# Optimization experiments

Measured on AMD Instinct MI355X. Metric: run time of the kernel, lower is better.

## Reference

```python
import jax, jax.numpy as jnp
import numpy as np
from jax import lax

EPS = 1e-6
CLAMP = 1e4


def _ln_last(x, w, b):
    # fp32 LayerNorm over last dim
    mu = jnp.mean(x, axis=-1, keepdims=True)
    var = jnp.mean(jnp.square(x - mu), axis=-1, keepdims=True)
    return (x - mu) * lax.rsqrt(var + EPS) * w + b


def _nan_clean(x):
    return jnp.nan_to_num(x, nan=0.0, posinf=CLAMP, neginf=-CLAMP)


def setup_inputs() -> dict:
    key = jax.random.key(0)
    B, C, H, W = 4, 256, 64, 64
    hid = 2 * C  # expand=2
    k = 3        # d_conv
    ks = jax.random.split(key, 12)
    s = 0.02
    return {
        "x": jax.random.normal(ks[0], (B, C, H, W), jnp.float32),
        "ln2d_w": jnp.ones((C,), jnp.float32),
        "ln2d_b": jnp.zeros((C,), jnp.float32),
        "inproj_w": jax.random.normal(ks[1], (C, C), jnp.float32) * s,
        "inproj_b": jnp.zeros((C,), jnp.float32),
        "dw2d_w": jax.random.normal(ks[2], (C, 3, 3), jnp.float32) * s,
        "dw2d_b": jnp.zeros((C,), jnp.float32),
        "ssm_ln_w": jnp.ones((C,), jnp.float32),
        "ssm_ln_b": jnp.zeros((C,), jnp.float32),
        "ssm_in_w": jax.random.normal(ks[3], (2 * hid, C), jnp.float32) * s,
        "ssm_in_b": jnp.zeros((2 * hid,), jnp.float32),
        "ssm_dw_w": jax.random.normal(ks[4], (hid, k), jnp.float32) * s,
        "ssm_dw_b": jnp.zeros((hid,), jnp.float32),
        "ssm_out_w": jax.random.normal(ks[5], (C, hid), jnp.float32) * s,
        "ssm_out_b": jnp.zeros((C,), jnp.float32),
        "outproj_w": jax.random.normal(ks[6], (C, C), jnp.float32) * s,
        "outproj_b": jnp.zeros((C,), jnp.float32),
    }


def reference(x, ln2d_w, ln2d_b, inproj_w, inproj_b, dw2d_w, dw2d_b,
              ssm_ln_w, ssm_ln_b, ssm_in_w, ssm_in_b, ssm_dw_w, ssm_dw_b,
              ssm_out_w, ssm_out_b, outproj_w, outproj_b):
    B, C, H, W = x.shape
    L = H * W

    # LN2d over channel dim (per-pixel LN on C)
    y = _ln_last(x.transpose(0, 2, 3, 1), ln2d_w, ln2d_b).transpose(0, 3, 1, 2)

    # 1x1 conv in_proj
    y = jnp.einsum('bchw,oc->bohw', y, inproj_w) + inproj_b[None, :, None, None]

    # depthwise 3x3 conv, SAME padding
    y = lax.conv_general_dilated(
        y, dw2d_w[:, None, :, :], (1, 1), ((1, 1), (1, 1)),
        dimension_numbers=('NCHW', 'OIHW', 'NCHW'),
        feature_group_count=C) + dw2d_b[None, :, None, None]

    # cross-scan: 4 routes (B,L,C)
    s0 = y.reshape(B, C, L).transpose(0, 2, 1)                      # row-major
    s1 = s0[:, ::-1]                                                # reversed
    s2 = y.transpose(0, 1, 3, 2).reshape(B, C, L).transpose(0, 2, 1)  # col-major
    s3 = s2[:, ::-1]
    s = jnp.concatenate([s0, s1, s2, s3], axis=0)  # (4B, L, C), shared SSM weights

    # MambaOrLite fallback: LN -> GLU -> depthwise conv1d -> out proj + residual
    r = _ln_last(s, ssm_ln_w, ssm_ln_b)
    r = r @ ssm_in_w.T + ssm_in_b                   # (4B, L, 2*hid)
    a, g = jnp.split(r, 2, axis=-1)
    r = a * jax.nn.sigmoid(g)                       # (4B, L, hid)
    r = r.transpose(0, 2, 1)                        # (4B, hid, L)
    hid = r.shape[1]
    k = ssm_dw_w.shape[-1]
    pad = ((k - 1) // 2, k // 2)
    r = lax.conv_general_dilated(
        r, ssm_dw_w[:, None, :], (1,), (pad,),
        dimension_numbers=('NCH', 'OIH', 'NCH'),
        feature_group_count=hid) + ssm_dw_b[None, :, None]
    r = r.transpose(0, 2, 1) @ ssm_out_w.T + ssm_out_b  # (4B, L, C)
    ys = _nan_clean(r) + s

    # cross-merge: average the 4 routes back to (B,C,H,W)
    y0, y1, y2, y3 = jnp.split(ys, 4, axis=0)
    m0 = y0.transpose(0, 2, 1).reshape(B, C, H, W)
    m1 = y1[:, ::-1].transpose(0, 2, 1).reshape(B, C, H, W)
    m2 = y2.transpose(0, 2, 1).reshape(B, C, W, H).transpose(0, 1, 3, 2)
    m3 = y3[:, ::-1].transpose(0, 2, 1).reshape(B, C, W, H).transpose(0, 1, 3, 2)
    m = (m0 + m1 + m2 + m3) * 0.25

    out = jnp.einsum('bchw,oc->bohw', m, outproj_w) + outproj_b[None, :, None, None]
    out = _nan_clean(out)
    return out + x
```

## Files before the change

kernel.cpp:

```cpp
#include <hip/hip_runtime.h>

typedef float f32x4 __attribute__((ext_vector_type(4)));
typedef __bf16 bf16x8 __attribute__((ext_vector_type(8)));
typedef unsigned short u16;
typedef unsigned int u32;

__device__ __forceinline__ float bf2f(u32 b) {
  u32 x = (b & 0xffffu) << 16;
  return __builtin_bit_cast(float, x);
}
__device__ __forceinline__ u16 f2bf(float f) {
  u32 x = __builtin_bit_cast(u32, f);
  x += 0x7fffu + ((x >> 16) & 1u);
  return (u16)(x >> 16);
}
__device__ __forceinline__ void gload16(const void* g, void* l) {
  __builtin_amdgcn_global_load_lds((__attribute__((address_space(1))) void*)g,
                                   (__attribute__((address_space(3))) void*)l,
                                   16, 0, 0);
}
__device__ __forceinline__ int xcd_swz(int bid, int nwg) {
  int per = nwg >> 3;
  return (bid & 7) * per + (bid >> 3);
}

__global__ __launch_bounds__(256, 2)
void k_ln2d_prep(const float* __restrict__ x, const float* __restrict__ lw,
                 const float* __restrict__ lb, u16* __restrict__ A,
                 const float* __restrict__ inproj_w, const float* __restrict__ ssm_in_w,
                 const float* __restrict__ ssm_out_w, const float* __restrict__ outproj_w,
                 const float* __restrict__ dw2d_w, const float* __restrict__ ssm_dw_w,
                 const float* __restrict__ ssm_dw_b, const float* __restrict__ ssm_out_b,
                 u16* __restrict__ w1b, u16* __restrict__ w2b, u16* __restrict__ w3b,
                 u16* __restrict__ w4b, float* __restrict__ cvec, float* __restrict__ wT9,
                 float* __restrict__ w02, float* __restrict__ w14) {
  __shared__ float T[256 * 65];
  __shared__ float ps1[4][64], ps2[4][64];
  __shared__ float mu[64], rsd[64];
  int bid = blockIdx.x, tid = threadIdx.x;
  if (bid >= 256) {
    int pb = bid - 256;
    if (pb < 512) {
      const float* s; u16* d; int base;
      if (pb < 256)      { s = ssm_in_w;  d = w2b; base = pb; }
      else if (pb < 384) { s = ssm_out_w; d = w3b; base = pb - 256; }
      else if (pb < 448) { s = inproj_w;  d = w1b; base = pb - 384; }
      else               { s = outproj_w; d = w4b; base = pb - 448; }
      int i = base * 1024 + tid * 4;
      float4 v = *(const float4*)&s[i];
      u32 a = (u32)f2bf(v.x) | ((u32)f2bf(v.y) << 16);
      u32 b = (u32)f2bf(v.z) | ((u32)f2bf(v.w) << 16);
      *(uint2*)&d[i] = make_uint2(a, b);
    } else if (pb == 512) {
      float s = ssm_out_b[tid];
      const float* wr = ssm_out_w + (size_t)tid * 512;
      #pragma unroll 8
      for (int k = 0; k < 512; ++k) s += ssm_dw_b[k] * wr[k];
      cvec[tid] = s;
    } else {
      #pragma unroll
      for (int j = 0; j < 9; ++j) wT9[j * 256 + tid] = dw2d_w[tid * 9 + j];
      #pragma unroll
      for (int q = 0; q < 2; ++q) {
        int c = tid + q * 256;
        w02[c] = ssm_dw_w[c * 3 + 0] + ssm_dw_w[c * 3 + 2];
        w14[c] = 4.f * ssm_dw_w[c * 3 + 1];
      }
    }
    return;
  }
  int wv = tid >> 6, lane = tid & 63;
  int cq = lane >> 4, p4 = (lane & 15) * 4;
  int n0 = bid * 64, bb = n0 >> 12, hw0 = n0 & 4095;
  const float* xb = x + ((size_t)bb << 20);
  float s0 = 0, s1 = 0, s2 = 0, s3 = 0;
  float q0 = 0, q1 = 0, q2 = 0, q3 = 0;
  #pragma unroll 4
  for (int i = 0; i < 16; ++i) {
    int c = wv * 64 + i * 4 + cq;
    float4 v = *(const float4*)&xb[((size_t)c << 12) + hw0 + p4];
    T[c * 65 + p4 + 0] = v.x; T[c * 65 + p4 + 1] = v.y;
    T[c * 65 + p4 + 2] = v.z; T[c * 65 + p4 + 3] = v.w;
    s0 += v.x; s1 += v.y; s2 += v.z; s3 += v.w;
    q0 += v.x * v.x; q1 += v.y * v.y; q2 += v.z * v.z; q3 += v.w * v.w;
  }
  #pragma unroll
  for (int off = 16; off < 64; off <<= 1) {
    s0 += __shfl_xor(s0, off); s1 += __shfl_xor(s1, off);
    s2 += __shfl_xor(s2, off); s3 += __shfl_xor(s3, off);
    q0 += __shfl_xor(q0, off); q1 += __shfl_xor(q1, off);
    q2 += __shfl_xor(q2, off); q3 += __shfl_xor(q3, off);
  }
  if (cq == 0) {
    ps1[wv][p4 + 0] = s0; ps1[wv][p4 + 1] = s1; ps1[wv][p4 + 2] = s2; ps1[wv][p4 + 3] = s3;
    ps2[wv][p4 + 0] = q0; ps2[wv][p4 + 1] = q1; ps2[wv][p4 + 2] = q2; ps2[wv][p4 + 3] = q3;
  }
  __syncthreads();
  if (tid < 64) {
    float S1 = ps1[0][tid] + ps1[1][tid] + ps1[2][tid] + ps1[3][tid];
    float S2 = ps2[0][tid] + ps2[1][tid] + ps2[2][tid] + ps2[3][tid];
    float m = S1 * (1.f / 256.f);
    float var = S2 * (1.f / 256.f) - m * m;
    mu[tid] = m;
    rsd[tid] = rsqrtf(var + 1e-6f);
  }
  __syncthreads();
  int c4b = (tid & 15) * 4, p2b = tid >> 4;
  #pragma unroll
  for (int cc = 0; cc < 4; ++cc) {
    int c4 = cc * 64 + c4b;
    float4 w4 = *(const float4*)&lw[c4];
    float4 g4 = *(const float4*)&lb[c4];
    #pragma unroll
    for (int i2 = 0; i2 < 4; ++i2) {
      int p2 = p2b + 16 * i2;
      float m = mu[p2], rs = rsd[p2];
      float o0 = (T[(c4 + 0) * 65 + p2] - m) * rs * w4.x + g4.x;
      float o1 = (T[(c4 + 1) * 65 + p2] - m) * rs * w4.y + g4.y;
      float o2 = (T[(c4 + 2) * 65 + p2] - m) * rs * w4.z + g4.z;
      float o3 = (T[(c4 + 3) * 65 + p2] - m) * rs * w4.w + g4.w;
      u32 a = (u32)f2bf(o0) | ((u32)f2bf(o1) << 16);
      u32 b = (u32)f2bf(o2) | ((u32)f2bf(o3) << 16);
      *(uint2*)&A[(size_t)(n0 + p2) * 256 + c4] = make_uint2(a, b);
    }
  }
}

__global__ __launch_bounds__(256)
void k_dw3x3_ln(const u16* __restrict__ Y1, const float* __restrict__ wT,
                const float* __restrict__ dwb, const float* __restrict__ lnw,
                const float* __restrict__ lnb, u16* __restrict__ Yc,
                u16* __restrict__ A) {
  int tid = threadIdx.x;
  int wg = xcd_swz(blockIdx.x, 4096);
  int n = wg * 4 + (tid >> 6);
  int lane = tid & 63;
  int c0 = lane * 4;
  int b = n >> 12, hw = n & 4095, h = hw >> 6, w = hw & 63;
  float4 b4 = *(const float4*)&dwb[c0];
  float a0 = b4.x, a1 = b4.y, a2 = b4.z, a3 = b4.w;
  #pragma unroll
  for (int ky = 0; ky < 3; ++ky) {
    int hh = h + ky - 1;
    if (hh < 0 || hh > 63) continue;
    #pragma unroll
    for (int kx = 0; kx < 3; ++kx) {
      int ww = w + kx - 1;
      if (ww < 0 || ww > 63) continue;
      size_t nn = ((size_t)b << 12) + (hh << 6) + ww;
      uint2 u = *(const uint2*)&Y1[nn * 256 + c0];
      float4 w4 = *(const float4*)&wT[(ky * 3 + kx) * 256 + c0];
      a0 += bf2f(u.x) * w4.x;
      a1 += bf2f(u.x >> 16) * w4.y;
      a2 += bf2f(u.y) * w4.z;
      a3 += bf2f(u.y >> 16) * w4.w;
    }
  }
  u32 p0 = (u32)f2bf(a0) | ((u32)f2bf(a1) << 16);
  u32 p1 = (u32)f2bf(a2) | ((u32)f2bf(a3) << 16);
  *(uint2*)&Yc[(size_t)n * 256 + c0] = make_uint2(p0, p1);
  float s1 = a0 + a1 + a2 + a3;
  float s2 = a0 * a0 + a1 * a1 + a2 * a2 + a3 * a3;
  #pragma unroll
  for (int off = 1; off < 64; off <<= 1) {
    s1 += __shfl_xor(s1, off);
    s2 += __shfl_xor(s2, off);
  }
  float m = s1 * (1.f / 256.f);
  float var = s2 * (1.f / 256.f) - m * m;
  float rs = rsqrtf(var + 1e-6f);
  float4 w4 = *(const float4*)&lnw[c0];
  float4 g4 = *(const float4*)&lnb[c0];
  float o0 = (a0 - m) * rs * w4.x + g4.x;
  float o1 = (a1 - m) * rs * w4.y + g4.y;
  float o2 = (a2 - m) * rs * w4.z + g4.z;
  float o3 = (a3 - m) * rs * w4.w + g4.w;
  u32 qa = (u32)f2bf(o0) | ((u32)f2bf(o1) << 16);
  u32 qb = (u32)f2bf(o2) | ((u32)f2bf(o3) << 16);
  *(uint2*)&A[(size_t)n * 256 + c0] = make_uint2(qa, qb);
}

template <int EPI, int NCT, bool RFAST>
__global__ __launch_bounds__(256, 4)
void k_gemm2(const u16* __restrict__ R, const u16* __restrict__ Cm,
             const float* __restrict__ bias, int K, int ldo,
             u16* __restrict__ outb, float* __restrict__ outf,
             const float* __restrict__ resf) {
  __shared__ u16 tR[2][64 * 32];
  __shared__ u16 tC[2][128 * 32];
  int tid = threadIdx.x, lane = tid & 63, wv = tid >> 6;
  int wg = xcd_swz(blockIdx.x, gridDim.x);
  int nRt = gridDim.x / NCT;
  int rt = RFAST ? (wg % nRt) : (wg / NCT);
  int ct = RFAST ? (wg / nRt) : (wg % NCT);
  int r0 = rt * 64, c0 = ct * 128;
  int fr = lane & 15, kc = lane >> 4;
  int sr = lane >> 2, sc = (lane & 3) * 8;
  f32x4 acc[4][2] = {};
  int nK = K >> 5;
  const u16* gR  = R  + (size_t)(r0 + wv * 16 + sr) * K + sc;
  const u16* gC0 = Cm + (size_t)(c0 + wv * 32 + sr) * K + sc;
  const u16* gC1 = Cm + (size_t)(c0 + wv * 32 + 16 + sr) * K + sc;
  auto STAGE = [&](int buf, int kt) {
    int k0 = kt * 32;
    gload16(gR + k0,  &tR[buf][wv * 16 * 32]);
    gload16(gC0 + k0, &tC[buf][(wv * 32) * 32]);
    gload16(gC1 + k0, &tC[buf][(wv * 32 + 16) * 32]);
  };
  auto COMPUTE = [&](int buf) {
    bf16x8 af[4], wf[2];
    #pragma unroll
    for (int m = 0; m < 4; ++m)
      af[m] = *(const bf16x8*)&tR[buf][(m * 16 + fr) * 32 + kc * 8];
    #pragma unroll
    for (int n = 0; n < 2; ++n)
      wf[n] = *(const bf16x8*)&tC[buf][(wv * 32 + n * 16 + fr) * 32 + kc * 8];
    #pragma unroll
    for (int m = 0; m < 4; ++m)
      #pragma unroll
      for (int n = 0; n < 2; ++n)
        acc[m][n] = __builtin_amdgcn_mfma_f32_16x16x32_bf16(af[m], wf[n], acc[m][n], 0, 0, 0);
  };
  STAGE(0, 0);
  __syncthreads();
  int cur = 0;
  for (int kt = 0; kt < nK - 1; ++kt) {
    STAGE(cur ^ 1, kt + 1);
    __builtin_amdgcn_sched_barrier(0);
    COMPUTE(cur);
    __syncthreads();
    cur ^= 1;
  }
  COMPUTE(cur);
  #pragma unroll
  for (int m = 0; m < 4; ++m) {
    #pragma unroll
    for (int n = 0; n < 2; ++n) {
      #pragma unroll
      for (int r = 0; r < 4; ++r) {
        float v = acc[m][n][r];
        if (EPI == 0) {
          int gn = r0 + m * 16 + kc * 4 + r;
          int go = c0 + wv * 32 + n * 16 + fr;
          outb[(size_t)gn * ldo + go] = f2bf(v + bias[go]);
        } else {
          int go = r0 + m * 16 + kc * 4 + r;
          int gn = c0 + wv * 32 + n * 16 + fr;
          int b = gn >> 12, hw = gn & 4095;
          size_t idx = (((size_t)(b * 256 + go)) << 12) + hw;
          float res = __builtin_nontemporal_load(&resf[idx]);
          __builtin_nontemporal_store(v + bias[go] + res, &outf[idx]);
        }
      }
    }
  }
}

__global__ __launch_bounds__(256, 2)
void k_gate2(const u16* __restrict__ A, const u16* __restrict__ W,
             const float* __restrict__ bias, u16* __restrict__ G) {
  __shared__ u16 tR[2][128 * 32];
  __shared__ u16 tCa[2][128 * 32];
  __shared__ u16 tCg[2][128 * 32];
  int tid = threadIdx.x, lane = tid & 63, wv = tid >> 6;
  int wg = xcd_swz(blockIdx.x, 512);
  int rt = wg >> 2, ot = wg & 3;
  int r0 = rt * 128, o0 = ot * 128;
  int wr = wv >> 1, wc = wv & 1;
  int fr = lane & 15, kc = lane >> 4;
  const int K = 256;
  f32x4 acca[4][4] = {}, accg[4][4] = {};
  auto STAGE = [&](int buf, int kt) {
    int k0 = kt * 32;
    #pragma unroll
    for (int i = 0; i < 2; ++i) {
      int s0 = wv * 128 + i * 64;
      int s = s0 + lane;
      int row = s >> 2, off = (s & 3) * 8;
      gload16(A + (size_t)(r0 + row) * K + k0 + off, &tR[buf][s0 * 8]);
      gload16(W + (size_t)(o0 + row) * K + k0 + off, &tCa[buf][s0 * 8]);
      gload16(W + (size_t)(512 + o0 + row) * K + k0 + off, &tCg[buf][s0 * 8]);
    }
  };
  auto COMPUTE = [&](int buf) {
    bf16x8 af[4], wa[4], wgf[4];
    #pragma unroll
    for (int m = 0; m < 4; ++m)
      af[m] = *(const bf16x8*)&tR[buf][(wr * 64 + m * 16 + fr) * 32 + kc * 8];
    #pragma unroll
    for (int n = 0; n < 4; ++n) {
      wa[n]  = *(const bf16x8*)&tCa[buf][(wc * 64 + n * 16 + fr) * 32 + kc * 8];
      wgf[n] = *(const bf16x8*)&tCg[buf][(wc * 64 + n * 16 + fr) * 32 + kc * 8];
    }
    #pragma unroll
    for (int m = 0; m < 4; ++m)
      #pragma unroll
      for (int n = 0; n < 4; ++n) {
        acca[m][n] = __builtin_amdgcn_mfma_f32_16x16x32_bf16(af[m], wa[n], acca[m][n], 0, 0, 0);
        accg[m][n] = __builtin_amdgcn_mfma_f32_16x16x32_bf16(af[m], wgf[n], accg[m][n], 0, 0, 0);
      }
  };
  STAGE(0, 0);
  __syncthreads();
  int cur = 0;
  for (int kt = 0; kt < 7; ++kt) {
    STAGE(cur ^ 1, kt + 1);
    __builtin_amdgcn_sched_barrier(0);
    COMPUTE(cur);
    __syncthreads();
    cur ^= 1;
  }
  COMPUTE(cur);
  #pragma unroll
  for (int m = 0; m < 4; ++m) {
    #pragma unroll
    for (int n = 0; n < 4; ++n) {
      #pragma unroll
      for (int r = 0; r < 4; ++r) {
        int gn = r0 + wr * 64 + m * 16 + kc * 4 + r;
        int go = o0 + wc * 64 + n * 16 + fr;
        float a = acca[m][n][r] + bias[go];
        float g = accg[m][n][r] + bias[512 + go];
        G[(size_t)gn * 512 + go] = f2bf(a / (1.f + expf(-g)));
      }
    }
  }
}

__global__ __launch_bounds__(256, 2)
void k_gemm_scan(const u16* __restrict__ G, const u16* __restrict__ W3,
                 const float* __restrict__ w02, const float* __restrict__ w14,
                 const float* __restrict__ cvec, const u16* __restrict__ Yc,
                 u16* __restrict__ M) {
  __shared__ u16 tR[2][32 * 32];
  __shared__ u16 tC[2][256 * 32];
  int tid = threadIdx.x, lane = tid & 63, wv = tid >> 6;
  int wg = xcd_swz(blockIdx.x, 512);
  int r0 = wg * 32;
  int fr = lane & 15, kc = lane >> 4;
  int zrow = tid >> 3;
  int zg = (tid & 7) * 4;
  int n = r0 + zrow;
  int b = n >> 12, hw = n & 4095, h = hw >> 6, w = hw & 63;
  int m = w * 64 + h;
  int mm1 = m - 1, mp1 = m + 1;
  size_t o_c = (size_t)n * 512 + zg;
  size_t o_p = (size_t)(hw > 0 ? n - 1 : n) * 512 + zg;
  size_t o_n = (size_t)(hw < 4095 ? n + 1 : n) * 512 + zg;
  size_t o_u = (size_t)(m > 0 ? ((b << 12) + ((mm1 & 63) << 6) + (mm1 >> 6)) : n) * 512 + zg;
  size_t o_d = (size_t)(m < 4095 ? ((b << 12) + ((mp1 & 63) << 6) + (mp1 >> 6)) : n) * 512 + zg;
  float mP = hw > 0 ? 1.f : 0.f, mN = hw < 4095 ? 1.f : 0.f;
  float mU = m > 0 ? 1.f : 0.f, mD = m < 4095 ? 1.f : 0.f;
  f32x4 acc[2][4] = {};
  auto STAGE_C = [&](int buf, int kt) {
    int k0 = kt * 32;
    #pragma unroll
    for (int i = 0; i < 4; ++i) {
      int s0 = wv * 256 + i * 64;
      int s = s0 + lane;
      int row = s >> 2, off = (s & 3) * 8;
      gload16(W3 + (size_t)row * 512 + k0 + off, &tC[buf][s0 * 8]);
    }
  };
  uint2 lc, lp, ln_, lu, ld;
  float4 va, vb;
  auto ZLOAD = [&](int kt) {
    int c = kt * 32 + zg;
    lc  = *(const uint2*)&G[o_c + (kt * 32)];
    lp  = *(const uint2*)&G[o_p + (kt * 32)];
    ln_ = *(const uint2*)&G[o_n + (kt * 32)];
    lu  = *(const uint2*)&G[o_u + (kt * 32)];
    ld  = *(const uint2*)&G[o_d + (kt * 32)];
    va = *(const float4*)&w02[c];
    vb = *(const float4*)&w14[c];
  };
  auto ZSTORE = [&](int buf) {
    float s_0 = mP * bf2f(lp.x) + mN * bf2f(ln_.x) + mU * bf2f(lu.x) + mD * bf2f(ld.x);
    float s_1 = mP * bf2f(lp.x >> 16) + mN * bf2f(ln_.x >> 16) + mU * bf2f(lu.x >> 16) + mD * bf2f(ld.x >> 16);
    float s_2 = mP * bf2f(lp.y) + mN * bf2f(ln_.y) + mU * bf2f(lu.y) + mD * bf2f(ld.y);
    float s_3 = mP * bf2f(lp.y >> 16) + mN * bf2f(ln_.y >> 16) + mU * bf2f(lu.y >> 16) + mD * bf2f(ld.y >> 16);
    float z0 = va.x * s_0 + vb.x * bf2f(lc.x);
    float z1 = va.y * s_1 + vb.y * bf2f(lc.x >> 16);
    float z2 = va.z * s_2 + vb.z * bf2f(lc.y);
    float z3 = va.w * s_3 + vb.w * bf2f(lc.y >> 16);
    u32 p0 = (u32)f2bf(z0) | ((u32)f2bf(z1) << 16);
    u32 p1 = (u32)f2bf(z2) | ((u32)f2bf(z3) << 16);
    *(uint2*)&tR[buf][zrow * 32 + zg] = make_uint2(p0, p1);
  };
  auto COMPUTE = [&](int buf) {
    bf16x8 af[2], wf[4];
    #pragma unroll
    for (int mi = 0; mi < 2; ++mi)
      af[mi] = *(const bf16x8*)&tR[buf][(mi * 16 + fr) * 32 + kc * 8];
    #pragma unroll
    for (int ni = 0; ni < 4; ++ni)
      wf[ni] = *(const bf16x8*)&tC[buf][(wv * 64 + ni * 16 + fr) * 32 + kc * 8];
    #pragma unroll
    for (int mi = 0; mi < 2; ++mi)
      #pragma unroll
      for (int ni = 0; ni < 4; ++ni)
        acc[mi][ni] = __builtin_amdgcn_mfma_f32_16x16x32_bf16(af[mi], wf[ni], acc[mi][ni], 0, 0, 0);
  };
  STAGE_C(0, 0);
  ZLOAD(0);
  ZSTORE(0);
  __syncthreads();
  int cur = 0;
  for (int kt = 0; kt < 15; ++kt) {
    ZLOAD(kt + 1);
    STAGE_C(cur ^ 1, kt + 1);
    COMPUTE(cur);
    ZSTORE(cur ^ 1);
    __syncthreads();
    cur ^= 1;
  }
  COMPUTE(cur);
  #pragma unroll
  for (int mi = 0; mi < 2; ++mi) {
    #pragma unroll
    for (int ni = 0; ni < 4; ++ni) {
      #pragma unroll
      for (int r = 0; r < 4; ++r) {
        int gn = r0 + mi * 16 + kc * 4 + r;
        int go = wv * 64 + ni * 16 + fr;
        size_t idx = (size_t)gn * 256 + go;
        M[idx] = f2bf(0.25f * acc[mi][ni][r] + cvec[go] + bf2f(Yc[idx]));
      }
    }
  }
}

extern "C" void kernel_launch(void* const* d_in, const int* in_sizes, int n_in,
                              void* d_out, int out_size, void* d_ws, size_t ws_size,
                              hipStream_t stream) {
  const float* x         = (const float*)d_in[0];
  const float* ln2d_w    = (const float*)d_in[1];
  const float* ln2d_b    = (const float*)d_in[2];
  const float* inproj_w  = (const float*)d_in[3];
  const float* inproj_b  = (const float*)d_in[4];
  const float* dw2d_w    = (const float*)d_in[5];
  const float* dw2d_b    = (const float*)d_in[6];
  const float* ssm_ln_w  = (const float*)d_in[7];
  const float* ssm_ln_b  = (const float*)d_in[8];
  const float* ssm_in_w  = (const float*)d_in[9];
  const float* ssm_in_b  = (const float*)d_in[10];
  const float* ssm_dw_w  = (const float*)d_in[11];
  const float* ssm_dw_b  = (const float*)d_in[12];
  const float* ssm_out_w = (const float*)d_in[13];
  const float* ssm_out_b = (const float*)d_in[14];
  const float* outproj_w = (const float*)d_in[15];
  const float* outproj_b = (const float*)d_in[16];
  float* out = (float*)d_out;

  char* ws = (char*)d_ws;
  size_t off = 0;
  auto take = [&](size_t bytes) -> char* {
    char* p = ws + off;
    off = (off + bytes + 255) & ~(size_t)255;
    return p;
  };
  u16* w1b    = (u16*)take(65536 * 2);
  u16* w2b    = (u16*)take(262144 * 2);
  u16* w3b    = (u16*)take(131072 * 2);
  u16* w4b    = (u16*)take(65536 * 2);
  float* cvec = (float*)take(256 * 4);
  float* wT9  = (float*)take(9 * 256 * 4);
  float* w02  = (float*)take(512 * 4);
  float* w14  = (float*)take(512 * 4);
  u16* Abuf   = (u16*)take((size_t)16384 * 256 * 2);
  u16* Y1     = (u16*)take((size_t)16384 * 256 * 2);
  u16* Yc     = (u16*)take((size_t)16384 * 256 * 2);
  u16* G      = (u16*)take((size_t)16384 * 512 * 2);
  (void)ws_size; (void)in_sizes; (void)n_in; (void)out_size;

  k_ln2d_prep<<<770, 256, 0, stream>>>(x, ln2d_w, ln2d_b, Abuf,
                                       inproj_w, ssm_in_w, ssm_out_w, outproj_w,
                                       dw2d_w, ssm_dw_w, ssm_dw_b, ssm_out_b,
                                       w1b, w2b, w3b, w4b, cvec, wT9, w02, w14);
  k_gemm2<0, 2, false><<<512, 256, 0, stream>>>(Abuf, w1b, inproj_b, 256, 256,
                                                Y1, nullptr, nullptr);
  k_dw3x3_ln<<<4096, 256, 0, stream>>>(Y1, wT9, dw2d_b, ssm_ln_w, ssm_ln_b, Yc, Abuf);
  k_gate2<<<512, 256, 0, stream>>>(Abuf, w2b, ssm_in_b, G);
  k_gemm_scan<<<512, 256, 0, stream>>>(G, w3b, w02, w14, cvec, Yc, Abuf);
  k_gemm2<2, 128, true><<<512, 256, 0, stream>>>(w4b, Abuf, outproj_b, 256, 0,
                                                 nullptr, out, x);
}
```

Measured before the change: 108.4 us.

## Fuse in_proj GEMM into LN2d kernel and out_proj GEMM into scan kernel

The in_proj GEMM moves into the LN2d kernel: normalized bf16 rows go into LDS and are multiplied right away with in_proj weights, which are converted from fp32 on the fly. The out_proj GEMM moves into the scan kernel, which keeps the merged tile in swizzled LDS and writes the NCHW output plus residual directly. This removes two launches and the global round trips of the intermediate activations. In exchange, weights are read from global without LDS staging (in_proj is also reconverted per block), LDS use per block rises, and the output stores change pattern.

```diff
diff --git a/kernel.cpp b/kernel.cpp
--- a/kernel.cpp
+++ b/kernel.cpp
@@ -23,35 +23,43 @@
   int per = nwg >> 3;
   return (bid & 7) * per + (bid >> 3);
 }
-
-__global__ __launch_bounds__(256, 2)
-void k_ln2d_prep(const float* __restrict__ x, const float* __restrict__ lw,
-                 const float* __restrict__ lb, u16* __restrict__ A,
-                 const float* __restrict__ inproj_w, const float* __restrict__ ssm_in_w,
-                 const float* __restrict__ ssm_out_w, const float* __restrict__ outproj_w,
-                 const float* __restrict__ dw2d_w, const float* __restrict__ ssm_dw_w,
-                 const float* __restrict__ ssm_dw_b, const float* __restrict__ ssm_out_b,
-                 u16* __restrict__ w1b, u16* __restrict__ w2b, u16* __restrict__ w3b,
-                 u16* __restrict__ w4b, float* __restrict__ cvec, float* __restrict__ wT9,
-                 float* __restrict__ w02, float* __restrict__ w14) {
-  __shared__ float T[256 * 65];
+__device__ __forceinline__ bf16x8 cvt8(const float* __restrict__ p) {
+  float4 lo = *(const float4*)p;
+  float4 hi = *(const float4*)(p + 4);
+  union { u16 e[8]; bf16x8 v; } u;
+  u.e[0] = f2bf(lo.x); u.e[1] = f2bf(lo.y); u.e[2] = f2bf(lo.z); u.e[3] = f2bf(lo.w);
+  u.e[4] = f2bf(hi.x); u.e[5] = f2bf(hi.y); u.e[6] = f2bf(hi.z); u.e[7] = f2bf(hi.w);
+  return u.v;
+}
+
+__global__ __launch_bounds__(256)
+void k_lnproj(const float* __restrict__ x, const float* __restrict__ lw,
+              const float* __restrict__ lb, const float* __restrict__ W1,
+              const float* __restrict__ inproj_b, u16* __restrict__ Y1,
+              const float* __restrict__ ssm_in_w, const float* __restrict__ ssm_out_w,
+              const float* __restrict__ outproj_w, const float* __restrict__ dw2d_w,
+              const float* __restrict__ ssm_dw_w, const float* __restrict__ ssm_dw_b,
+              const float* __restrict__ ssm_out_b,
+              u16* __restrict__ w2b, u16* __restrict__ w3b, u16* __restrict__ w4b,
+              float* __restrict__ cvec, float* __restrict__ wT9,
+              float* __restrict__ w02, float* __restrict__ w14) {
+  __shared__ u16 sA[64 * 264];
   __shared__ float ps1[4][64], ps2[4][64];
   __shared__ float mu[64], rsd[64];
   int bid = blockIdx.x, tid = threadIdx.x;
   if (bid >= 256) {
     int pb = bid - 256;
-    if (pb < 512) {
+    if (pb < 448) {
       const float* s; u16* d; int base;
       if (pb < 256)      { s = ssm_in_w;  d = w2b; base = pb; }
       else if (pb < 384) { s = ssm_out_w; d = w3b; base = pb - 256; }
-      else if (pb < 448) { s = inproj_w;  d = w1b; base = pb - 384; }
-      else               { s = outproj_w; d = w4b; base = pb - 448; }
+      else               { s = outproj_w; d = w4b; base = pb - 384; }
       int i = base * 1024 + tid * 4;
       float4 v = *(const float4*)&s[i];
       u32 a = (u32)f2bf(v.x) | ((u32)f2bf(v.y) << 16);
       u32 b = (u32)f2bf(v.z) | ((u32)f2bf(v.w) << 16);
       *(uint2*)&d[i] = make_uint2(a, b);
-    } else if (pb == 512) {
+    } else if (pb == 448) {
       float s = ssm_out_b[tid];
       const float* wr = ssm_out_w + (size_t)tid * 512;
       #pragma unroll 8
@@ -73,14 +81,14 @@
   int cq = lane >> 4, p4 = (lane & 15) * 4;
   int n0 = bid * 64, bb = n0 >> 12, hw0 = n0 & 4095;
   const float* xb = x + ((size_t)bb << 20);
+  float4 xv[16];
   float s0 = 0, s1 = 0, s2 = 0, s3 = 0;
   float q0 = 0, q1 = 0, q2 = 0, q3 = 0;
-  #pragma unroll 4
+  #pragma unroll
   for (int i = 0; i < 16; ++i) {
     int c = wv * 64 + i * 4 + cq;
     float4 v = *(const float4*)&xb[((size_t)c << 12) + hw0 + p4];
-    T[c * 65 + p4 + 0] = v.x; T[c * 65 + p4 + 1] = v.y;
-    T[c * 65 + p4 + 2] = v.z; T[c * 65 + p4 + 3] = v.w;
+    xv[i] = v;
     s0 += v.x; s1 += v.y; s2 += v.z; s3 += v.w;
     q0 += v.x * v.x; q1 += v.y * v.y; q2 += v.z * v.z; q3 += v.w * v.w;
   }
@@ -105,23 +113,43 @@
     rsd[tid] = rsqrtf(var + 1e-6f);
   }
   __syncthreads();
-  int c4b = (tid & 15) * 4, p2b = tid >> 4;
-  #pragma unroll
-  for (int cc = 0; cc < 4; ++cc) {
-    int c4 = cc * 64 + c4b;
-    float4 w4 = *(const float4*)&lw[c4];
-    float4 g4 = *(const float4*)&lb[c4];
-    #pragma unroll
-    for (int i2 = 0; i2 < 4; ++i2) {
-      int p2 = p2b + 16 * i2;
-      float m = mu[p2], rs = rsd[p2];
-      float o0 = (T[(c4 + 0) * 65 + p2] - m) * rs * w4.x + g4.x;
-      float o1 = (T[(c4 + 1) * 65 + p2] - m) * rs * w4.y + g4.y;
-      float o2 = (T[(c4 + 2) * 65 + p2] - m) * rs * w4.z + g4.z;
-      float o3 = (T[(c4 + 3) * 65 + p2] - m) * rs * w4.w + g4.w;
-      u32 a = (u32)f2bf(o0) | ((u32)f2bf(o1) << 16);
-      u32 b = (u32)f2bf(o2) | ((u32)f2bf(o3) << 16);
-      *(uint2*)&A[(size_t)(n0 + p2) * 256 + c4] = make_uint2(a, b);
+  #pragma unroll
+  for (int i = 0; i < 16; ++i) {
+    int c = wv * 64 + i * 4 + cq;
+    float wc = lw[c], bc = lb[c];
+    float4 v = xv[i];
+    sA[(p4 + 0) * 264 + c] = f2bf((v.x - mu[p4 + 0]) * rsd[p4 + 0] * wc + bc);
+    sA[(p4 + 1) * 264 + c] = f2bf((v.y - mu[p4 + 1]) * rsd[p4 + 1] * wc + bc);
+    sA[(p4 + 2) * 264 + c] = f2bf((v.z - mu[p4 + 2]) * rsd[p4 + 2] * wc + bc);
+    sA[(p4 + 3) * 264 + c] = f2bf((v.w - mu[p4 + 3]) * rsd[p4 + 3] * wc + bc);
+  }
+  __syncthreads();
+  int fr = lane & 15, kc = lane >> 4;
+  f32x4 acc[4][4] = {};
+  #pragma unroll 2
+  for (int kt = 0; kt < 8; ++kt) {
+    bf16x8 af[4];
+    #pragma unroll
+    for (int m = 0; m < 4; ++m)
+      af[m] = *(const bf16x8*)&sA[(m * 16 + fr) * 264 + kt * 32 + kc * 8];
+    #pragma unroll
+    for (int n = 0; n < 4; ++n) {
+      bf16x8 wf = cvt8(W1 + (size_t)(wv * 64 + n * 16 + fr) * 256 + kt * 32 + kc * 8);
+      #pragma unroll
+      for (int m = 0; m < 4; ++m)
+        acc[m][n] = __builtin_amdgcn_mfma_f32_16x16x32_bf16(af[m], wf, acc[m][n], 0, 0, 0);
+    }
+  }
+  #pragma unroll
+  for (int m = 0; m < 4; ++m) {
+    #pragma unroll
+    for (int n = 0; n < 4; ++n) {
+      #pragma unroll
+      for (int r = 0; r < 4; ++r) {
+        int gn = n0 + m * 16 + kc * 4 + r;
+        int go = wv * 64 + n * 16 + fr;
+        Y1[(size_t)gn * 256 + go] = f2bf(acc[m][n][r] + inproj_b[go]);
+      }
     }
   }
 }
@@ -178,82 +206,6 @@
   u32 qa = (u32)f2bf(o0) | ((u32)f2bf(o1) << 16);
   u32 qb = (u32)f2bf(o2) | ((u32)f2bf(o3) << 16);
   *(uint2*)&A[(size_t)n * 256 + c0] = make_uint2(qa, qb);
-}
-
-template <int EPI, int NCT, bool RFAST>
-__global__ __launch_bounds__(256, 4)
-void k_gemm2(const u16* __restrict__ R, const u16* __restrict__ Cm,
-             const float* __restrict__ bias, int K, int ldo,
-             u16* __restrict__ outb, float* __restrict__ outf,
-             const float* __restrict__ resf) {
-  __shared__ u16 tR[2][64 * 32];
-  __shared__ u16 tC[2][128 * 32];
-  int tid = threadIdx.x, lane = tid & 63, wv = tid >> 6;
-  int wg = xcd_swz(blockIdx.x, gridDim.x);
-  int nRt = gridDim.x / NCT;
-  int rt = RFAST ? (wg % nRt) : (wg / NCT);
-  int ct = RFAST ? (wg / nRt) : (wg % NCT);
-  int r0 = rt * 64, c0 = ct * 128;
-  int fr = lane & 15, kc = lane >> 4;
-  int sr = lane >> 2, sc = (lane & 3) * 8;
-  f32x4 acc[4][2] = {};
-  int nK = K >> 5;
-  const u16* gR  = R  + (size_t)(r0 + wv * 16 + sr) * K + sc;
-  const u16* gC0 = Cm + (size_t)(c0 + wv * 32 + sr) * K + sc;
-  const u16* gC1 = Cm + (size_t)(c0 + wv * 32 + 16 + sr) * K + sc;
-  auto STAGE = [&](int buf, int kt) {
-    int k0 = kt * 32;
-    gload16(gR + k0,  &tR[buf][wv * 16 * 32]);
-    gload16(gC0 + k0, &tC[buf][(wv * 32) * 32]);
-    gload16(gC1 + k0, &tC[buf][(wv * 32 + 16) * 32]);
-  };
-  auto COMPUTE = [&](int buf) {
-    bf16x8 af[4], wf[2];
-    #pragma unroll
-    for (int m = 0; m < 4; ++m)
-      af[m] = *(const bf16x8*)&tR[buf][(m * 16 + fr) * 32 + kc * 8];
-    #pragma unroll
-    for (int n = 0; n < 2; ++n)
-      wf[n] = *(const bf16x8*)&tC[buf][(wv * 32 + n * 16 + fr) * 32 + kc * 8];
-    #pragma unroll
-    for (int m = 0; m < 4; ++m)
-      #pragma unroll
-      for (int n = 0; n < 2; ++n)
-        acc[m][n] = __builtin_amdgcn_mfma_f32_16x16x32_bf16(af[m], wf[n], acc[m][n], 0, 0, 0);
-  };
-  STAGE(0, 0);
-  __syncthreads();
-  int cur = 0;
-  for (int kt = 0; kt < nK - 1; ++kt) {
-    STAGE(cur ^ 1, kt + 1);
-    __builtin_amdgcn_sched_barrier(0);
-    COMPUTE(cur);
-    __syncthreads();
-    cur ^= 1;
-  }
-  COMPUTE(cur);
-  #pragma unroll
-  for (int m = 0; m < 4; ++m) {
-    #pragma unroll
-    for (int n = 0; n < 2; ++n) {
-      #pragma unroll
-      for (int r = 0; r < 4; ++r) {
-        float v = acc[m][n][r];
-        if (EPI == 0) {
-          int gn = r0 + m * 16 + kc * 4 + r;
-          int go = c0 + wv * 32 + n * 16 + fr;
-          outb[(size_t)gn * ldo + go] = f2bf(v + bias[go]);
-        } else {
-          int go = r0 + m * 16 + kc * 4 + r;
-          int gn = c0 + wv * 32 + n * 16 + fr;
-          int b = gn >> 12, hw = gn & 4095;
-          size_t idx = (((size_t)(b * 256 + go)) << 12) + hw;
-          float res = __builtin_nontemporal_load(&resf[idx]);
-          __builtin_nontemporal_store(v + bias[go] + res, &outf[idx]);
-        }
-      }
-    }
-  }
 }
 
 __global__ __launch_bounds__(256, 2)
@@ -328,12 +280,14 @@
 }
 
 __global__ __launch_bounds__(256, 2)
-void k_gemm_scan(const u16* __restrict__ G, const u16* __restrict__ W3,
-                 const float* __restrict__ w02, const float* __restrict__ w14,
-                 const float* __restrict__ cvec, const u16* __restrict__ Yc,
-                 u16* __restrict__ M) {
+void k_scan_out(const u16* __restrict__ G, const u16* __restrict__ W3,
+                const float* __restrict__ w02, const float* __restrict__ w14,
+                const float* __restrict__ cvec, const u16* __restrict__ Yc,
+                const u16* __restrict__ W4, const float* __restrict__ outb,
+                const float* __restrict__ xres, float* __restrict__ out) {
   __shared__ u16 tR[2][32 * 32];
   __shared__ u16 tC[2][256 * 32];
+  __shared__ u16 sM[32 * 256];
   int tid = threadIdx.x, lane = tid & 63, wv = tid >> 6;
   int wg = xcd_swz(blockIdx.x, 512);
   int r0 = wg * 32;
@@ -421,10 +375,47 @@
     for (int ni = 0; ni < 4; ++ni) {
       #pragma unroll
       for (int r = 0; r < 4; ++r) {
-        int gn = r0 + mi * 16 + kc * 4 + r;
+        int row = mi * 16 + kc * 4 + r;
         int go = wv * 64 + ni * 16 + fr;
-        size_t idx = (size_t)gn * 256 + go;
-        M[idx] = f2bf(0.25f * acc[mi][ni][r] + cvec[go] + bf2f(Yc[idx]));
+        float mval = 0.25f * acc[mi][ni][r] + cvec[go] +
+                     bf2f(Yc[(size_t)(r0 + row) * 256 + go]);
+        u32 ba = ((u32)(row * 512 + go * 2)) ^ ((u32)(row & 7) << 4);
+        *(u16*)((char*)sM + ba) = f2bf(mval);
+      }
+    }
+  }
+  __syncthreads();
+  f32x4 acc2[4][2] = {};
+  #pragma unroll 2
+  for (int kt = 0; kt < 8; ++kt) {
+    bf16x8 af2[4], bfv[2];
+    #pragma unroll
+    for (int mi = 0; mi < 4; ++mi)
+      af2[mi] = *(const bf16x8*)&W4[(size_t)(wv * 64 + mi * 16 + fr) * 256 + kt * 32 + kc * 8];
+    #pragma unroll
+    for (int ni = 0; ni < 2; ++ni) {
+      int pos = ni * 16 + fr;
+      u32 ba = ((u32)(pos * 512 + (kt * 32 + kc * 8) * 2)) ^ ((u32)(pos & 7) << 4);
+      bfv[ni] = *(const bf16x8*)((const char*)sM + ba);
+    }
+    #pragma unroll
+    for (int mi = 0; mi < 4; ++mi)
+      #pragma unroll
+      for (int ni = 0; ni < 2; ++ni)
+        acc2[mi][ni] = __builtin_amdgcn_mfma_f32_16x16x32_bf16(af2[mi], bfv[ni], acc2[mi][ni], 0, 0, 0);
+  }
+  int bb = r0 >> 12, hwb = r0 & 4095;
+  #pragma unroll
+  for (int mi = 0; mi < 4; ++mi) {
+    #pragma unroll
+    for (int ni = 0; ni < 2; ++ni) {
+      #pragma unroll
+      for (int r = 0; r < 4; ++r) {
+        int o = wv * 64 + mi * 16 + kc * 4 + r;
+        int pos = ni * 16 + fr;
+        size_t idx = (((size_t)(bb * 256 + o)) << 12) + hwb + pos;
+        float res = __builtin_nontemporal_load(&xres[idx]);
+        __builtin_nontemporal_store(acc2[mi][ni][r] + outb[o] + res, &out[idx]);
       }
     }
   }
@@ -459,7 +450,6 @@
     off = (off + bytes + 255) & ~(size_t)255;
     return p;
   };
-  u16* w1b    = (u16*)take(65536 * 2);
   u16* w2b    = (u16*)take(262144 * 2);
   u16* w3b    = (u16*)take(131072 * 2);
   u16* w4b    = (u16*)take(65536 * 2);
@@ -473,15 +463,12 @@
   u16* G      = (u16*)take((size_t)16384 * 512 * 2);
   (void)ws_size; (void)in_sizes; (void)n_in; (void)out_size;
 
-  k_ln2d_prep<<<770, 256, 0, stream>>>(x, ln2d_w, ln2d_b, Abuf,
-                                       inproj_w, ssm_in_w, ssm_out_w, outproj_w,
-                                       dw2d_w, ssm_dw_w, ssm_dw_b, ssm_out_b,
-                                       w1b, w2b, w3b, w4b, cvec, wT9, w02, w14);
-  k_gemm2<0, 2, false><<<512, 256, 0, stream>>>(Abuf, w1b, inproj_b, 256, 256,
-                                                Y1, nullptr, nullptr);
+  k_lnproj<<<706, 256, 0, stream>>>(x, ln2d_w, ln2d_b, inproj_w, inproj_b, Y1,
+                                    ssm_in_w, ssm_out_w, outproj_w, dw2d_w,
+                                    ssm_dw_w, ssm_dw_b, ssm_out_b,
+                                    w2b, w3b, w4b, cvec, wT9, w02, w14);
   k_dw3x3_ln<<<4096, 256, 0, stream>>>(Y1, wT9, dw2d_b, ssm_ln_w, ssm_ln_b, Yc, Abuf);
   k_gate2<<<512, 256, 0, stream>>>(Abuf, w2b, ssm_in_b, G);
-  k_gemm_scan<<<512, 256, 0, stream>>>(G, w3b, w02, w14, cvec, Yc, Abuf);
-  k_gemm2<2, 128, true><<<512, 256, 0, stream>>>(w4b, Abuf, outproj_b, 256, 0,
-                                                 nullptr, out, x);
-}
+  k_scan_out<<<512, 256, 0, stream>>>(G, w3b, w02, w14, cvec, Yc,
+                                      w4b, outproj_b, x, out);
+}
```

Result: faster. 105.9 us (-2.3%).
